# Kernel optimization log

Hardware: AMD Instinct MI355X
Metric: run time of the kernel (lower is better)

## Reference

```python
import jax, jax.numpy as jnp
import numpy as np

B, S, D_MODEL, H, D_KV = 16, 512, 768, 12, 64
EPS = 1e-6
ROPE_THETA = 10000.0


def rms_norm(x, w, eps=EPS):
    var = jnp.mean(jnp.square(x.astype(jnp.float32)), axis=-1, keepdims=True)
    return w * (x * jax.lax.rsqrt(var + eps))


def rotate_half(x):
    x1, x2 = jnp.split(x, 2, axis=-1)
    return jnp.concatenate([-x2, x1], axis=-1)


def build_rope(position_ids, inv_freq):
    # position_ids: [B,S] int; inv_freq: [d_kv/2]
    freqs = position_ids[:, :, None].astype(jnp.float32) * inv_freq[None, None, :]  # [B,S,d/2]
    emb = jnp.concatenate([freqs, freqs], axis=-1)  # [B,S,d_kv]
    return jnp.cos(emb), jnp.sin(emb)


def shape_heads(x, n_heads, d_kv):
    b, s, _ = x.shape
    return x.reshape(b, s, n_heads, d_kv).transpose(0, 2, 1, 3)  # [b,h,s,d]


def attend(h, norm_w, wq, wk, wv, wo, mask, cos=None, sin=None):
    # h: [b,s,d_model]; mask: [b,h,s,s] additive
    normed = rms_norm(h, norm_w)
    q = shape_heads(normed @ wq.T, H, D_KV)
    k = shape_heads(normed @ wk.T, H, D_KV)
    v = shape_heads(normed @ wv.T, H, D_KV)
    if cos is not None:
        c = cos[:, None, :, :]
        s = sin[:, None, :, :]
        q = q * c + rotate_half(q) * s
        k = k * c + rotate_half(k) * s
    # NOTE: kernel has no 1/sqrt(d) scaling
    scores = jnp.einsum('bhqd,bhkd->bhqk', q, k) + mask
    p = jax.nn.softmax(scores, axis=-1)
    out = jnp.einsum('bhqk,bhkd->bhqd', p, v)
    b, _, s, _ = out.shape
    out = out.transpose(0, 2, 1, 3).reshape(b, s, H * D_KV)
    return h + out @ wo.T


def setup_inputs() -> dict:
    key = jax.random.key(0)
    ks = jax.random.split(key, 12)
    scale = 1.0 / np.sqrt(D_MODEL)
    inp = {
        'hidden_states': jax.random.normal(ks[0], (B, S, D_MODEL), dtype=jnp.float32),
        'position_ids': jnp.broadcast_to(jnp.arange(S, dtype=jnp.int32)[None, :], (B, S)),
        'attention_mask': jnp.broadcast_to(
            jnp.where(jnp.arange(S)[None, :] <= jnp.arange(S)[:, None], 0.0, -1e9).astype(jnp.float32),
            (B, H, S, S)) + 0.0,
        'group_time_mask': jnp.zeros((S, H, B, B), dtype=jnp.float32),
        't_q': jax.random.normal(ks[1], (H * D_KV, D_MODEL), dtype=jnp.float32) * scale,
        't_k': jax.random.normal(ks[2], (H * D_KV, D_MODEL), dtype=jnp.float32) * scale,
        't_v': jax.random.normal(ks[3], (H * D_KV, D_MODEL), dtype=jnp.float32) * scale,
        't_o': jax.random.normal(ks[4], (D_MODEL, H * D_KV), dtype=jnp.float32) * scale,
        't_norm_w': jnp.ones((D_MODEL,), dtype=jnp.float32),
        'g_q': jax.random.normal(ks[5], (H * D_KV, D_MODEL), dtype=jnp.float32) * scale,
        'g_k': jax.random.normal(ks[6], (H * D_KV, D_MODEL), dtype=jnp.float32) * scale,
        'g_v': jax.random.normal(ks[7], (H * D_KV, D_MODEL), dtype=jnp.float32) * scale,
        'g_o': jax.random.normal(ks[8], (D_MODEL, H * D_KV), dtype=jnp.float32) * scale,
        'g_norm_w': jnp.ones((D_MODEL,), dtype=jnp.float32),
        'inv_freq': (1.0 / ROPE_THETA ** (jnp.arange(0, D_KV, 2, dtype=jnp.float32) / D_KV)),
    }
    return inp


def reference(hidden_states, position_ids, attention_mask, group_time_mask,
              t_q, t_k, t_v, t_o, t_norm_w,
              g_q, g_k, g_v, g_o, g_norm_w, inv_freq):
    cos, sin = build_rope(position_ids, inv_freq)
    h = attend(hidden_states, t_norm_w, t_q, t_k, t_v, t_o, attention_mask, cos, sin)
    h = h.transpose(1, 0, 2)  # [S,B,D]: group attention attends across groups
    h = attend(h, g_norm_w, g_q, g_k, g_v, g_o, group_time_mask)
    return h.transpose(1, 0, 2)
```

## Files before the change

### kernel.cpp

```cpp
#include <hip/hip_runtime.h>

#define DM   768
#define QKVN 2304
#define SQ   512
#define NB   16
#define NH   12

typedef unsigned short u16;
typedef _Float16 h16;
typedef _Float16 h16x8 __attribute__((ext_vector_type(8)));
typedef float f32x4 __attribute__((ext_vector_type(4)));

__device__ __forceinline__ u16 f2h(float f) {
  h16 h = (h16)f;
  return __builtin_bit_cast(u16, h);
}
__device__ __forceinline__ float h2f(u16 u) {
  return (float)__builtin_bit_cast(h16, u);
}
__device__ __forceinline__ void gload_lds16(const void* g, void* l) {
  __builtin_amdgcn_global_load_lds((__attribute__((address_space(1))) void*)(g),
                                   (__attribute__((address_space(3))) void*)(l), 16, 0, 0);
}

struct WPtrs { const float* s[8]; u16* d[8]; };
__global__ __launch_bounds__(256) void prep_k(WPtrs P, const float* __restrict__ invf,
                                              float* __restrict__ tab,
                                              const float* __restrict__ x,
                                              const float* __restrict__ tnw, const float* __restrict__ gnw,
                                              u16* __restrict__ xh, float* __restrict__ rs1) {
  const int bid = blockIdx.x, tid = threadIdx.x;
  if (bid < 4608) {
    int w = bid / 576;
    int i = ((bid % 576) * 256 + tid) * 4;
    float4 v = *reinterpret_cast<const float4*>(P.s[w] + i);
    if (w < 3 || (w >= 4 && w < 7)) {
      const float* nw = (w < 3) ? tnw : gnw;
      int k = i % 768;
      float4 f = *reinterpret_cast<const float4*>(nw + k);
      v.x *= f.x; v.y *= f.y; v.z *= f.z; v.w *= f.w;
    }
    ushort4 o;
    o.x = f2h(v.x); o.y = f2h(v.y); o.z = f2h(v.z); o.w = f2h(v.w);
    *reinterpret_cast<ushort4*>(P.d[w] + i) = o;
  } else if (bid < 4672) {
    int i = (bid - 4608) * 256 + tid;
    int pos = i >> 5, j = i & 31;
    float a = (float)pos * invf[j];
    float s, c;
    sincosf(a, &s, &c);
    tab[i * 2] = c; tab[i * 2 + 1] = s;
  } else {
    int wv = tid >> 6, lane = tid & 63;
    size_t t = (size_t)(bid - 4672) * 4 + wv;
    const float* row = x + t * DM;
    float4 v[3];
    float ss = 0.f;
#pragma unroll
    for (int i = 0; i < 3; i++) {
      v[i] = *reinterpret_cast<const float4*>(row + (lane + 64 * i) * 4);
      ss += v[i].x * v[i].x + v[i].y * v[i].y + v[i].z * v[i].z + v[i].w * v[i].w;
    }
#pragma unroll
    for (int d = 1; d < 64; d <<= 1) ss += __shfl_xor(ss, d);
    u16* orow = xh + t * DM;
#pragma unroll
    for (int i = 0; i < 3; i++) {
      int c = (lane + 64 * i) * 4;
      ushort4 o;
      o.x = f2h(v[i].x); o.y = f2h(v[i].y); o.z = f2h(v[i].z); o.w = f2h(v[i].w);
      *reinterpret_cast<ushort4*>(orow + c) = o;
    }
    if (lane == 0) rs1[t] = rsqrtf(ss * (1.0f / 768.f) + 1e-6f);
  }
}

__global__ __launch_bounds__(256) void rs2_k(const u16* __restrict__ x, float* __restrict__ rs2) {
  int wv = threadIdx.x >> 6, lane = threadIdx.x & 63;
  size_t t = (size_t)blockIdx.x * 4 + wv;
  const u16* row = x + t * DM;
  float ss = 0.f;
#pragma unroll
  for (int i = 0; i < 3; i++) {
    ushort4 rw = *reinterpret_cast<const ushort4*>(row + (lane + 64 * i) * 4);
    float a = h2f(rw.x), b = h2f(rw.y), c = h2f(rw.z), d = h2f(rw.w);
    ss += a * a + b * b + c * c + d * d;
  }
#pragma unroll
  for (int d = 1; d < 64; d <<= 1) ss += __shfl_xor(ss, d);
  if (lane == 0) rs2[t] = rsqrtf(ss * (1.0f / 768.f) + 1e-6f);
}

template <int CMODE, bool ROPE, int PERM, bool VT, bool RS>
__global__ __launch_bounds__(256, 3) void gemm_k(const u16* __restrict__ A, const u16* __restrict__ W, int N,
                                              void* __restrict__ C, const void* __restrict__ resid,
                                              const int* __restrict__ pids, const float* __restrict__ tab,
                                              u16* __restrict__ vt, const float* __restrict__ rsb) {
  __shared__ __align__(16) char L[3 * 16384];
  const int tid = threadIdx.x, w = tid >> 6, lane = tid & 63;
  const int wr = w >> 1, wc = w & 1;
  const int nbn = gridDim.y;
  int nf = blockIdx.y * gridDim.x + blockIdx.x;
  int nwg = gridDim.x * nbn;
  int swv = (nf & 7) * (nwg >> 3) + (nf >> 3);
  const int bm = swv / nbn;
  const int bnb = swv % nbn;
  const int l15 = lane & 15, l4 = lane >> 4;
  f32x4 acc[4][4] = {};

  const int r0 = tid >> 2, k40 = tid & 3;
  const int k4s = k40 ^ ((r0 >> 1) & 3);
  const size_t aA0 = (size_t)(bm * 128 + r0) * 1536 + k4s * 16;
  const size_t aA1 = (size_t)(bm * 128 + r0 + 64) * 1536 + k4s * 16;
  const size_t aB0 = (size_t)(bnb * 128 + r0) * 1536 + k4s * 16;
  const size_t aB1 = (size_t)(bnb * 128 + r0 + 64) * 1536 + k4s * 16;
  const int dc0 = tid * 16, dc1 = dc0 + 4096;
  const char* Ab = (const char*)A;
  const char* Wb = (const char*)W;

#define STAGE(T64, Q) do { \
    gload_lds16(Ab + aA0 + (T64), L + (Q) * 16384 + dc0); \
    gload_lds16(Ab + aA1 + (T64), L + (Q) * 16384 + dc1); \
    gload_lds16(Wb + aB0 + (T64), L + (Q) * 16384 + 8192 + dc0); \
    gload_lds16(Wb + aB1 + (T64), L + (Q) * 16384 + 8192 + dc1); \
  } while (0)

  int obA[4], obB[4];
#pragma unroll
  for (int i = 0; i < 4; i++) {
    int rowA = wr * 64 + i * 16 + l15;
    obA[i] = rowA * 64 + ((l4 ^ ((rowA >> 1) & 3)) * 16);
    int rowB = wc * 64 + i * 16 + l15;
    obB[i] = 8192 + rowB * 64 + ((l4 ^ ((rowB >> 1) & 3)) * 16);
  }

  STAGE(0, 0); STAGE(64, 1);
  asm volatile("s_waitcnt vmcnt(4)" ::: "memory");
  __builtin_amdgcn_sched_barrier(0);
  __builtin_amdgcn_s_barrier();
  __builtin_amdgcn_sched_barrier(0);

#pragma unroll
  for (int to = 0; to < 8; ++to) {
#pragma unroll
    for (int ti = 0; ti < 3; ++ti) {
      const int t = to * 3 + ti;
      const int tn = (t + 2 < 24) ? (t + 2) : 23;
      STAGE(tn * 64, (t + 2) % 3);
      const char* bq = L + (t % 3) * 16384;
      h16x8 am[4], bn[4];
#pragma unroll
      for (int i = 0; i < 4; i++) am[i] = *reinterpret_cast<const h16x8*>(bq + obA[i]);
#pragma unroll
      for (int j = 0; j < 4; j++) bn[j] = *reinterpret_cast<const h16x8*>(bq + obB[j]);
      __builtin_amdgcn_s_setprio(1);
#pragma unroll
      for (int i = 0; i < 4; i++)
#pragma unroll
        for (int j = 0; j < 4; j++)
          acc[i][j] = __builtin_amdgcn_mfma_f32_16x16x32_f16(am[i], bn[j], acc[i][j], 0, 0, 0);
      __builtin_amdgcn_s_setprio(0);
      asm volatile("s_waitcnt vmcnt(4)" ::: "memory");
      __builtin_amdgcn_sched_barrier(0);
      __builtin_amdgcn_s_barrier();
      __builtin_amdgcn_sched_barrier(0);
    }
  }
#undef STAGE
  asm volatile("s_waitcnt vmcnt(0)" ::: "memory");

  if (RS) {
#pragma unroll
    for (int i = 0; i < 4; i++) {
      int row0 = bm * 128 + wr * 64 + i * 16 + l4 * 4;
#pragma unroll
      for (int r = 0; r < 4; r++) {
        float s = rsb[row0 + r];
#pragma unroll
        for (int j = 0; j < 4; j++) acc[i][j][r] *= s;
      }
    }
  }

  if (VT && bnb >= 12) {
#pragma unroll
    for (int i = 0; i < 4; i++) {
      int row0 = bm * 128 + wr * 64 + i * 16 + l4 * 4;
      int b = row0 >> 9, s0 = row0 & 511;
#pragma unroll
      for (int j = 0; j < 4; j++) {
        int vcol = bnb * 128 + wc * 64 + j * 16 + l15 - 1536;
        int hh = vcol >> 6, dd = vcol & 63;
        u16* dst = vt + (((size_t)(b * NH + hh) * 64 + dd) << 9) + s0;
        ushort4 o;
        o.x = f2h(acc[i][j][0]); o.y = f2h(acc[i][j][1]);
        o.z = f2h(acc[i][j][2]); o.w = f2h(acc[i][j][3]);
        *reinterpret_cast<ushort4*>(dst) = o;
      }
    }
    return;
  }

  if (ROPE && bnb < 12) {
#pragma unroll
    for (int i = 0; i < 4; i++) {
      int row0 = bm * 128 + wr * 64 + i * 16 + l4 * 4;
#pragma unroll
      for (int r = 0; r < 4; r++) {
        int pos = pids[row0 + r];
        const float* tb = tab + pos * 64;
#pragma unroll
        for (int j = 0; j < 2; j++) {
          float2 cs = *reinterpret_cast<const float2*>(tb + 2 * (j * 16 + l15));
          float x1 = acc[i][j][r], x2 = acc[i][j + 2][r];
          acc[i][j][r]     = x1 * cs.x - x2 * cs.y;
          acc[i][j + 2][r] = x2 * cs.x + x1 * cs.y;
        }
      }
    }
  }
#pragma unroll
  for (int i = 0; i < 4; i++) {
    int row0 = bm * 128 + wr * 64 + i * 16 + l4 * 4;
#pragma unroll
    for (int j = 0; j < 4; j++) {
      int col = bnb * 128 + wc * 64 + j * 16 + l15;
#pragma unroll
      for (int r = 0; r < 4; r++) {
        int rr = row0 + r;
        int orow = (PERM == 0) ? rr : (PERM == 1) ? ((rr & 511) * 16 + (rr >> 9))
                                                  : ((rr & 15) * 512 + (rr >> 4));
        size_t idx = (size_t)orow * N + col;
        float v = acc[i][j][r];
        if (CMODE == 0)      ((u16*)C)[idx] = f2h(v);
        else if (CMODE == 1) ((u16*)C)[idx] = f2h(v + h2f(((const u16*)resid)[idx]));
        else                 ((float*)C)[idx] = v + h2f(((const u16*)resid)[idx]);
      }
    }
  }
}

__global__ __launch_bounds__(256) void attn1_k(const u16* __restrict__ qkv, const u16* __restrict__ vt,
                                               u16* __restrict__ O) {
  __shared__ __align__(16) char L[2][32768];
  __shared__ __align__(16) char Pl[4][4096];
  int nf = blockIdx.y * 8 + blockIdx.x;
  int swv = (nf & 7) * 192 + (nf >> 3);
  const int qt = swv & 7;
  const int bh = swv >> 3;
  const int b = bh / NH, h = bh % NH;
  const int tid = threadIdx.x, w = tid >> 6, lane = tid & 63;
  const int l15 = lane & 15, l4 = lane >> 4;
  const size_t qoff = ((size_t)(b * SQ + qt * 64 + w * 16 + l15)) * QKVN + h * 64;
  h16x8 qf[2];
  qf[0] = *reinterpret_cast<const h16x8*>(qkv + qoff + 8 * l4);
  qf[1] = *reinterpret_cast<const h16x8*>(qkv + qoff + 32 + 8 * l4);
  f32x4 acco[4] = {};
  float mrun[4] = {-3e38f, -3e38f, -3e38f, -3e38f};
  float lrun[4] = {0.f, 0.f, 0.f, 0.f};
  const int qrow = qt * 64 + w * 16 + l4 * 4;
  const int nkt = (qt >> 1) + 1;

  const u16* Kg = qkv + (size_t)b * SQ * QKVN + DM + h * 64;
  const int rK0 = tid >> 3;
  const size_t aK0 = (size_t)rK0 * QKVN + (size_t)(((tid & 7) ^ (rK0 & 7)) * 8);
  const u16* Vg = vt + (size_t)bh * 64 * SQ;
  const int dV0 = tid >> 4;
  const size_t aV0 = (size_t)dV0 * SQ + (size_t)(((tid & 15) ^ (dV0 & 15)) * 8);
  const int dst0 = tid * 16;

#define STAGE1(KT, BUF) do { \
    _Pragma("unroll") \
    for (int e = 0; e < 4; e++) \
      gload_lds16(Kg + aK0 + (size_t)e * (32 * QKVN) + (size_t)(KT) * (128 * QKVN), \
                  L[BUF] + dst0 + e * 4096); \
    _Pragma("unroll") \
    for (int e = 0; e < 4; e++) \
      gload_lds16(Vg + aV0 + e * (16 * SQ) + (KT) * 128, \
                  L[BUF] + 16384 + dst0 + e * 4096); \
  } while (0)

  STAGE1(0, 0);
  asm volatile("s_waitcnt vmcnt(0)" ::: "memory");
  __builtin_amdgcn_sched_barrier(0);
  __builtin_amdgcn_s_barrier();
  __builtin_amdgcn_sched_barrier(0);

  for (int kt = 0; kt < nkt; ++kt) {
    const int cur = kt & 1;
    if (kt + 1 < nkt) STAGE1(kt + 1, cur ^ 1);
    const char* Kb = L[cur];
    const char* Vb = L[cur] + 16384;
    f32x4 sc[8] = {};
    __builtin_amdgcn_s_setprio(1);
#pragma unroll
    for (int kk = 0; kk < 2; kk++) {
#pragma unroll
      for (int j = 0; j < 8; j++) {
        int row = j * 16 + l15;
        int off = row * 128 + (((kk * 4 + l4) ^ (row & 7)) * 16);
        h16x8 kf = *reinterpret_cast<const h16x8*>(Kb + off);
        sc[j] = __builtin_amdgcn_mfma_f32_16x16x32_f16(qf[kk], kf, sc[j], 0, 0, 0);
      }
    }
    __builtin_amdgcn_s_setprio(0);
    float pv[8][4];
#pragma unroll
    for (int j = 0; j < 8; j++)
#pragma unroll
      for (int r = 0; r < 4; r++) pv[j][r] = sc[j][r];
    if (kt == nkt - 1) {
#pragma unroll
      for (int r = 0; r < 4; r++) {
        int q = qrow + r;
#pragma unroll
        for (int j = 0; j < 8; j++) {
          int key = kt * 128 + j * 16 + l15;
          if (key > q) pv[j][r] = -1e30f;
        }
      }
    }
    float al[4];
#pragma unroll
    for (int r = 0; r < 4; r++) {
      float t0 = fmaxf(fmaxf(pv[0][r], pv[1][r]), fmaxf(pv[2][r], pv[3][r]));
      float t1 = fmaxf(fmaxf(pv[4][r], pv[5][r]), fmaxf(pv[6][r], pv[7][r]));
      float tm = fmaxf(t0, t1);
      tm = fmaxf(tm, __shfl_xor(tm, 1)); tm = fmaxf(tm, __shfl_xor(tm, 2));
      tm = fmaxf(tm, __shfl_xor(tm, 4)); tm = fmaxf(tm, __shfl_xor(tm, 8));
      float mn = fmaxf(mrun[r], tm);
      al[r] = __expf(mrun[r] - mn);
      mrun[r] = mn;
      float ts = 0.f;
#pragma unroll
      for (int j = 0; j < 8; j++) { float p = __expf(pv[j][r] - mn); pv[j][r] = p; ts += p; }
      ts += __shfl_xor(ts, 1); ts += __shfl_xor(ts, 2); ts += __shfl_xor(ts, 4); ts += __shfl_xor(ts, 8);
      lrun[r] = lrun[r] * al[r] + ts;
    }
#pragma unroll
    for (int j = 0; j < 4; j++)
#pragma unroll
      for (int r = 0; r < 4; r++) acco[j][r] *= al[r];
    char* pw = Pl[w];
#pragma unroll
    for (int r = 0; r < 4; r++) {
      int q = l4 * 4 + r;
#pragma unroll
      for (int j = 0; j < 8; j++) {
        int cw = j * 2 + (l15 >> 3);
        int byte = q * 256 + ((cw ^ (q & 15)) * 16) + (l15 & 7) * 2;
        *(u16*)(pw + byte) = f2h(pv[j][r]);
      }
    }
    asm volatile("s_waitcnt lgkmcnt(0)" ::: "memory");
    __builtin_amdgcn_sched_barrier(0);
    __builtin_amdgcn_s_setprio(1);
#pragma unroll
    for (int kk = 0; kk < 4; kk++) {
      h16x8 pa = *reinterpret_cast<const h16x8*>(pw + l15 * 256 + (((kk * 4 + l4) ^ l15) * 16));
#pragma unroll
      for (int j = 0; j < 4; j++) {
        int d = j * 16 + l15;
        int voff = d * 256 + (((kk * 4 + l4) ^ (d & 15)) * 16);
        h16x8 vf = *reinterpret_cast<const h16x8*>(Vb + voff);
        acco[j] = __builtin_amdgcn_mfma_f32_16x16x32_f16(pa, vf, acco[j], 0, 0, 0);
      }
    }
    __builtin_amdgcn_s_setprio(0);
    asm volatile("s_waitcnt vmcnt(0)" ::: "memory");
    __builtin_amdgcn_sched_barrier(0);
    __builtin_amdgcn_s_barrier();
    __builtin_amdgcn_sched_barrier(0);
  }
#undef STAGE1
#pragma unroll
  for (int r = 0; r < 4; r++) {
    float inv = 1.f / lrun[r];
    size_t orow = ((size_t)(b * SQ + qrow + r)) * DM + h * 64;
#pragma unroll
    for (int j = 0; j < 4; j++) O[orow + j * 16 + l15] = f2h(acco[j][r] * inv);
  }
}

__global__ __launch_bounds__(256) void attn2_k(const u16* __restrict__ qkv, const float* __restrict__ gmask,
                                               u16* __restrict__ O) {
  __shared__ float Pl[4][16][16];
  __shared__ float Vl[4][16][68];
  const int tid = threadIdx.x, w = tid >> 6, lane = tid & 63;
  const int idx = blockIdx.x * 4 + w;
  const int s = idx / NH, h = idx % NH;
  const int l15 = lane & 15, l4 = lane >> 4;
  const size_t base = ((size_t)(s * 16 + l15)) * QKVN + h * 64;
  h16x8 qf0 = *reinterpret_cast<const h16x8*>(qkv + base + 8 * l4);
  h16x8 qf1 = *reinterpret_cast<const h16x8*>(qkv + base + 32 + 8 * l4);
  h16x8 kf0 = *reinterpret_cast<const h16x8*>(qkv + base + DM + 8 * l4);
  h16x8 kf1 = *reinterpret_cast<const h16x8*>(qkv + base + DM + 32 + 8 * l4);
  f32x4 sc = {};
  sc = __builtin_amdgcn_mfma_f32_16x16x32_f16(qf0, kf0, sc, 0, 0, 0);
  sc = __builtin_amdgcn_mfma_f32_16x16x32_f16(qf1, kf1, sc, 0, 0, 0);
  {
    int key = lane >> 2, d0 = (lane & 3) * 16;
    const u16* vsrc = qkv + ((size_t)(s * 16 + key)) * QKVN + 2 * DM + h * 64 + d0;
#pragma unroll
    for (int i = 0; i < 16; i += 4) {
      ushort4 vv = *reinterpret_cast<const ushort4*>(vsrc + i);
      Vl[w][key][d0 + i + 0] = h2f(vv.x);
      Vl[w][key][d0 + i + 1] = h2f(vv.y);
      Vl[w][key][d0 + i + 2] = h2f(vv.z);
      Vl[w][key][d0 + i + 3] = h2f(vv.w);
    }
  }
  const float* gm = gmask + ((size_t)s * NH + h) * 256;
#pragma unroll
  for (int r = 0; r < 4; r++) {
    float v = sc[r] + gm[(l4 * 4 + r) * 16 + l15];
    float mx = v;
    mx = fmaxf(mx, __shfl_xor(mx, 1)); mx = fmaxf(mx, __shfl_xor(mx, 2));
    mx = fmaxf(mx, __shfl_xor(mx, 4)); mx = fmaxf(mx, __shfl_xor(mx, 8));
    float p = __expf(v - mx);
    float su = p;
    su += __shfl_xor(su, 1); su += __shfl_xor(su, 2); su += __shfl_xor(su, 4); su += __shfl_xor(su, 8);
    Pl[w][l4 * 4 + r][l15] = p / su;
  }
  asm volatile("s_waitcnt lgkmcnt(0)" ::: "memory");
  __builtin_amdgcn_sched_barrier(0);
  const int q = lane >> 2, d0 = (lane & 3) * 16;
  float o[16] = {};
#pragma unroll
  for (int key = 0; key < 16; key++) {
    float pp = Pl[w][q][key];
#pragma unroll
    for (int dd = 0; dd < 16; dd += 4) {
      float4 vv = *reinterpret_cast<const float4*>(&Vl[w][key][d0 + dd]);
      o[dd + 0] += pp * vv.x; o[dd + 1] += pp * vv.y; o[dd + 2] += pp * vv.z; o[dd + 3] += pp * vv.w;
    }
  }
  u16* orow = O + ((size_t)(s * 16 + q)) * DM + h * 64 + d0;
#pragma unroll
  for (int i = 0; i < 16; i += 4) {
    ushort4 ov;
    ov.x = f2h(o[i]); ov.y = f2h(o[i + 1]); ov.z = f2h(o[i + 2]); ov.w = f2h(o[i + 3]);
    *reinterpret_cast<ushort4*>(orow + i) = ov;
  }
}

extern "C" void kernel_launch(void* const* d_in, const int* in_sizes, int n_in,
                              void* d_out, int out_size, void* d_ws, size_t ws_size,
                              hipStream_t stream) {
  const float* hidden = (const float*)d_in[0];
  const int*   pids   = (const int*)d_in[1];
  const float* gmask  = (const float*)d_in[3];
  const float* tq = (const float*)d_in[4];
  const float* tk = (const float*)d_in[5];
  const float* tv = (const float*)d_in[6];
  const float* to_ = (const float*)d_in[7];
  const float* tnw = (const float*)d_in[8];
  const float* gq = (const float*)d_in[9];
  const float* gk = (const float*)d_in[10];
  const float* gv = (const float*)d_in[11];
  const float* go = (const float*)d_in[12];
  const float* gnw = (const float*)d_in[13];
  const float* invf = (const float*)d_in[14];
  float* out = (float*)d_out;
  char* ws = (char*)d_ws;

  u16*   wq1    = (u16*)(ws);
  u16*   wo1    = (u16*)(ws + 3538944);
  u16*   wq2    = (u16*)(ws + 4718592);
  u16*   wo2    = (u16*)(ws + 8257536);
  float* tab    = (float*)(ws + 9437184);
  u16*   xh     = (u16*)(ws + 9568256);
  u16*   obuf   = (u16*)(ws + 22151168);
  u16*   h1     = (u16*)(ws + 34734080);
  u16*   qkv    = (u16*)(ws + 59899904);
  u16*   vt     = (u16*)(ws + 97648640);
  float* rs1    = (float*)(ws + 110231552);
  float* rs2    = (float*)(ws + 110264320);

  const int WN = 768 * 768;
  WPtrs P;
  P.s[0] = tq;  P.d[0] = wq1;
  P.s[1] = tk;  P.d[1] = wq1 + WN;
  P.s[2] = tv;  P.d[2] = wq1 + 2 * WN;
  P.s[3] = to_; P.d[3] = wo1;
  P.s[4] = gq;  P.d[4] = wq2;
  P.s[5] = gk;  P.d[5] = wq2 + WN;
  P.s[6] = gv;  P.d[6] = wq2 + 2 * WN;
  P.s[7] = go;  P.d[7] = wo2;

  prep_k<<<6720, 256, 0, stream>>>(P, invf, tab, hidden, tnw, gnw, xh, rs1);
  gemm_k<0, true, 0, true, true><<<dim3(64, 18), 256, 0, stream>>>(xh, wq1, QKVN, qkv, nullptr, pids, tab, vt, rs1);
  attn1_k<<<dim3(8, 192), 256, 0, stream>>>(qkv, vt, obuf);
  gemm_k<1, false, 0, false, false><<<dim3(64, 6), 256, 0, stream>>>(obuf, wo1, DM, h1, xh, nullptr, nullptr, nullptr, nullptr);

  rs2_k<<<2048, 256, 0, stream>>>(h1, rs2);
  gemm_k<0, false, 1, false, true><<<dim3(64, 18), 256, 0, stream>>>(h1, wq2, QKVN, qkv, nullptr, nullptr, nullptr, nullptr, rs2);
  attn2_k<<<1536, 256, 0, stream>>>(qkv, gmask, obuf);
  gemm_k<2, false, 2, false, false><<<dim3(64, 6), 256, 0, stream>>>(obuf, wo2, DM, out, h1, nullptr, nullptr, nullptr, nullptr);
}
```

Before: 197.0 us.

## Halve GEMM M-tile and fuse second RMS-norm sum-of-squares into O-projection epilogue

Shrinks the GEMM block tile from 128x128 to 64x128, doubling grid size and raising the occupancy bound to 4 blocks per CU. The standalone rs2 reduction kernel is removed: the first output-projection GEMM accumulates per-row sums of squares via shuffles and atomicAdd into a buffer zeroed in prep_k. The following QKV GEMM then computes rsqrt from that buffer. This cuts one launch and a full pass over h1, at the cost of atomics and more redundant weight-tile loads from the smaller M tile.

Result: slower. 219.0 us (+11.2%).

```diff
diff --git a/kernel.cpp b/kernel.cpp
--- a/kernel.cpp
+++ b/kernel.cpp
@@ -28,7 +28,8 @@
                                               float* __restrict__ tab,
                                               const float* __restrict__ x,
                                               const float* __restrict__ tnw, const float* __restrict__ gnw,
-                                              u16* __restrict__ xh, float* __restrict__ rs1) {
+                                              u16* __restrict__ xh, float* __restrict__ rs1,
+                                              float* __restrict__ ssq) {
   const int bid = blockIdx.x, tid = threadIdx.x;
   if (bid < 4608) {
     int w = bid / 576;
@@ -50,6 +51,7 @@
     float s, c;
     sincosf(a, &s, &c);
     tab[i * 2] = c; tab[i * 2 + 1] = s;
+    if (i < 8192) ssq[i] = 0.f;
   } else {
     int wv = tid >> 6, lane = tid & 63;
     size_t t = (size_t)(bid - 4672) * 4 + wv;
@@ -75,28 +77,13 @@
   }
 }
 
-__global__ __launch_bounds__(256) void rs2_k(const u16* __restrict__ x, float* __restrict__ rs2) {
-  int wv = threadIdx.x >> 6, lane = threadIdx.x & 63;
-  size_t t = (size_t)blockIdx.x * 4 + wv;
-  const u16* row = x + t * DM;
-  float ss = 0.f;
-#pragma unroll
-  for (int i = 0; i < 3; i++) {
-    ushort4 rw = *reinterpret_cast<const ushort4*>(row + (lane + 64 * i) * 4);
-    float a = h2f(rw.x), b = h2f(rw.y), c = h2f(rw.z), d = h2f(rw.w);
-    ss += a * a + b * b + c * c + d * d;
-  }
-#pragma unroll
-  for (int d = 1; d < 64; d <<= 1) ss += __shfl_xor(ss, d);
-  if (lane == 0) rs2[t] = rsqrtf(ss * (1.0f / 768.f) + 1e-6f);
-}
-
-template <int CMODE, bool ROPE, int PERM, bool VT, bool RS>
-__global__ __launch_bounds__(256, 3) void gemm_k(const u16* __restrict__ A, const u16* __restrict__ W, int N,
+template <int CMODE, bool ROPE, int PERM, bool VT, int RSMODE, bool SSQ>
+__global__ __launch_bounds__(256, 4) void gemm_k(const u16* __restrict__ A, const u16* __restrict__ W, int N,
                                               void* __restrict__ C, const void* __restrict__ resid,
                                               const int* __restrict__ pids, const float* __restrict__ tab,
-                                              u16* __restrict__ vt, const float* __restrict__ rsb) {
-  __shared__ __align__(16) char L[3 * 16384];
+                                              u16* __restrict__ vt, const float* __restrict__ rsb,
+                                              float* __restrict__ ssq) {
+  __shared__ __align__(16) char L[3 * 12288];
   const int tid = threadIdx.x, w = tid >> 6, lane = tid & 63;
   const int wr = w >> 1, wc = w & 1;
   const int nbn = gridDim.y;
@@ -106,36 +93,37 @@
   const int bm = swv / nbn;
   const int bnb = swv % nbn;
   const int l15 = lane & 15, l4 = lane >> 4;
-  f32x4 acc[4][4] = {};
+  f32x4 acc[2][4] = {};
 
   const int r0 = tid >> 2, k40 = tid & 3;
   const int k4s = k40 ^ ((r0 >> 1) & 3);
-  const size_t aA0 = (size_t)(bm * 128 + r0) * 1536 + k4s * 16;
-  const size_t aA1 = (size_t)(bm * 128 + r0 + 64) * 1536 + k4s * 16;
+  const size_t aA0 = (size_t)(bm * 64 + r0) * 1536 + k4s * 16;
   const size_t aB0 = (size_t)(bnb * 128 + r0) * 1536 + k4s * 16;
   const size_t aB1 = (size_t)(bnb * 128 + r0 + 64) * 1536 + k4s * 16;
-  const int dc0 = tid * 16, dc1 = dc0 + 4096;
+  const int dcA = tid * 16, dcB0 = 4096 + tid * 16, dcB1 = 8192 + tid * 16;
   const char* Ab = (const char*)A;
   const char* Wb = (const char*)W;
 
 #define STAGE(T64, Q) do { \
-    gload_lds16(Ab + aA0 + (T64), L + (Q) * 16384 + dc0); \
-    gload_lds16(Ab + aA1 + (T64), L + (Q) * 16384 + dc1); \
-    gload_lds16(Wb + aB0 + (T64), L + (Q) * 16384 + 8192 + dc0); \
-    gload_lds16(Wb + aB1 + (T64), L + (Q) * 16384 + 8192 + dc1); \
+    gload_lds16(Ab + aA0 + (T64), L + (Q) * 12288 + dcA); \
+    gload_lds16(Wb + aB0 + (T64), L + (Q) * 12288 + dcB0); \
+    gload_lds16(Wb + aB1 + (T64), L + (Q) * 12288 + dcB1); \
   } while (0)
 
-  int obA[4], obB[4];
-#pragma unroll
-  for (int i = 0; i < 4; i++) {
-    int rowA = wr * 64 + i * 16 + l15;
+  int obA[2], obB[4];
+#pragma unroll
+  for (int i = 0; i < 2; i++) {
+    int rowA = wr * 32 + i * 16 + l15;
     obA[i] = rowA * 64 + ((l4 ^ ((rowA >> 1) & 3)) * 16);
-    int rowB = wc * 64 + i * 16 + l15;
-    obB[i] = 8192 + rowB * 64 + ((l4 ^ ((rowB >> 1) & 3)) * 16);
+  }
+#pragma unroll
+  for (int j = 0; j < 4; j++) {
+    int rowB = wc * 64 + j * 16 + l15;
+    obB[j] = 4096 + rowB * 64 + ((l4 ^ ((rowB >> 1) & 3)) * 16);
   }
 
   STAGE(0, 0); STAGE(64, 1);
-  asm volatile("s_waitcnt vmcnt(4)" ::: "memory");
+  asm volatile("s_waitcnt vmcnt(3)" ::: "memory");
   __builtin_amdgcn_sched_barrier(0);
   __builtin_amdgcn_s_barrier();
   __builtin_amdgcn_sched_barrier(0);
@@ -147,20 +135,20 @@
       const int t = to * 3 + ti;
       const int tn = (t + 2 < 24) ? (t + 2) : 23;
       STAGE(tn * 64, (t + 2) % 3);
-      const char* bq = L + (t % 3) * 16384;
-      h16x8 am[4], bn[4];
-#pragma unroll
-      for (int i = 0; i < 4; i++) am[i] = *reinterpret_cast<const h16x8*>(bq + obA[i]);
+      const char* bq = L + (t % 3) * 12288;
+      h16x8 am[2], bn[4];
+#pragma unroll
+      for (int i = 0; i < 2; i++) am[i] = *reinterpret_cast<const h16x8*>(bq + obA[i]);
 #pragma unroll
       for (int j = 0; j < 4; j++) bn[j] = *reinterpret_cast<const h16x8*>(bq + obB[j]);
       __builtin_amdgcn_s_setprio(1);
 #pragma unroll
-      for (int i = 0; i < 4; i++)
+      for (int i = 0; i < 2; i++)
 #pragma unroll
         for (int j = 0; j < 4; j++)
           acc[i][j] = __builtin_amdgcn_mfma_f32_16x16x32_f16(am[i], bn[j], acc[i][j], 0, 0, 0);
       __builtin_amdgcn_s_setprio(0);
-      asm volatile("s_waitcnt vmcnt(4)" ::: "memory");
+      asm volatile("s_waitcnt vmcnt(3)" ::: "memory");
       __builtin_amdgcn_sched_barrier(0);
       __builtin_amdgcn_s_barrier();
       __builtin_amdgcn_sched_barrier(0);
@@ -169,13 +157,14 @@
 #undef STAGE
   asm volatile("s_waitcnt vmcnt(0)" ::: "memory");
 
-  if (RS) {
-#pragma unroll
-    for (int i = 0; i < 4; i++) {
-      int row0 = bm * 128 + wr * 64 + i * 16 + l4 * 4;
+  if (RSMODE) {
+#pragma unroll
+    for (int i = 0; i < 2; i++) {
+      int row0 = bm * 64 + wr * 32 + i * 16 + l4 * 4;
 #pragma unroll
       for (int r = 0; r < 4; r++) {
-        float s = rsb[row0 + r];
+        float s = (RSMODE == 1) ? rsb[row0 + r]
+                                : rsqrtf(rsb[row0 + r] * (1.0f / 768.f) + 1e-6f);
 #pragma unroll
         for (int j = 0; j < 4; j++) acc[i][j][r] *= s;
       }
@@ -184,8 +173,8 @@
 
   if (VT && bnb >= 12) {
 #pragma unroll
-    for (int i = 0; i < 4; i++) {
-      int row0 = bm * 128 + wr * 64 + i * 16 + l4 * 4;
+    for (int i = 0; i < 2; i++) {
+      int row0 = bm * 64 + wr * 32 + i * 16 + l4 * 4;
       int b = row0 >> 9, s0 = row0 & 511;
 #pragma unroll
       for (int j = 0; j < 4; j++) {
@@ -203,8 +192,8 @@
 
   if (ROPE && bnb < 12) {
 #pragma unroll
-    for (int i = 0; i < 4; i++) {
-      int row0 = bm * 128 + wr * 64 + i * 16 + l4 * 4;
+    for (int i = 0; i < 2; i++) {
+      int row0 = bm * 64 + wr * 32 + i * 16 + l4 * 4;
 #pragma unroll
       for (int r = 0; r < 4; r++) {
         int pos = pids[row0 + r];
@@ -220,21 +209,28 @@
     }
   }
 #pragma unroll
-  for (int i = 0; i < 4; i++) {
-    int row0 = bm * 128 + wr * 64 + i * 16 + l4 * 4;
-#pragma unroll
-    for (int j = 0; j < 4; j++) {
-      int col = bnb * 128 + wc * 64 + j * 16 + l15;
-#pragma unroll
-      for (int r = 0; r < 4; r++) {
-        int rr = row0 + r;
-        int orow = (PERM == 0) ? rr : (PERM == 1) ? ((rr & 511) * 16 + (rr >> 9))
-                                                  : ((rr & 15) * 512 + (rr >> 4));
+  for (int i = 0; i < 2; i++) {
+    int row0 = bm * 64 + wr * 32 + i * 16 + l4 * 4;
+#pragma unroll
+    for (int r = 0; r < 4; r++) {
+      int rr = row0 + r;
+      int orow = (PERM == 0) ? rr : (PERM == 1) ? ((rr & 511) * 16 + (rr >> 9))
+                                                : ((rr & 15) * 512 + (rr >> 4));
+      float sq = 0.f;
+#pragma unroll
+      for (int j = 0; j < 4; j++) {
+        int col = bnb * 128 + wc * 64 + j * 16 + l15;
         size_t idx = (size_t)orow * N + col;
         float v = acc[i][j][r];
         if (CMODE == 0)      ((u16*)C)[idx] = f2h(v);
-        else if (CMODE == 1) ((u16*)C)[idx] = f2h(v + h2f(((const u16*)resid)[idx]));
+        else if (CMODE == 1) { v += h2f(((const u16*)resid)[idx]); ((u16*)C)[idx] = f2h(v); }
         else                 ((float*)C)[idx] = v + h2f(((const u16*)resid)[idx]);
+        if (SSQ) sq += v * v;
+      }
+      if (SSQ) {
+        sq += __shfl_xor(sq, 1); sq += __shfl_xor(sq, 2);
+        sq += __shfl_xor(sq, 4); sq += __shfl_xor(sq, 8);
+        if (l15 == 0) atomicAdd(&ssq[rr], sq);
       }
     }
   }
@@ -475,7 +471,7 @@
   u16*   qkv    = (u16*)(ws + 59899904);
   u16*   vt     = (u16*)(ws + 97648640);
   float* rs1    = (float*)(ws + 110231552);
-  float* rs2    = (float*)(ws + 110264320);
+  float* ssq    = (float*)(ws + 110264320);
 
   const int WN = 768 * 768;
   WPtrs P;
@@ -488,13 +484,12 @@
   P.s[6] = gv;  P.d[6] = wq2 + 2 * WN;
   P.s[7] = go;  P.d[7] = wo2;
 
-  prep_k<<<6720, 256, 0, stream>>>(P, invf, tab, hidden, tnw, gnw, xh, rs1);
-  gemm_k<0, true, 0, true, true><<<dim3(64, 18), 256, 0, stream>>>(xh, wq1, QKVN, qkv, nullptr, pids, tab, vt, rs1);
+  prep_k<<<6720, 256, 0, stream>>>(P, invf, tab, hidden, tnw, gnw, xh, rs1, ssq);
+  gemm_k<0, true, 0, true, 1, false><<<dim3(128, 18), 256, 0, stream>>>(xh, wq1, QKVN, qkv, nullptr, pids, tab, vt, rs1, nullptr);
   attn1_k<<<dim3(8, 192), 256, 0, stream>>>(qkv, vt, obuf);
-  gemm_k<1, false, 0, false, false><<<dim3(64, 6), 256, 0, stream>>>(obuf, wo1, DM, h1, xh, nullptr, nullptr, nullptr, nullptr);
-
-  rs2_k<<<2048, 256, 0, stream>>>(h1, rs2);
-  gemm_k<0, false, 1, false, true><<<dim3(64, 18), 256, 0, stream>>>(h1, wq2, QKVN, qkv, nullptr, nullptr, nullptr, nullptr, rs2);
+  gemm_k<1, false, 0, false, 0, true><<<dim3(128, 6), 256, 0, stream>>>(obuf, wo1, DM, h1, xh, nullptr, nullptr, nullptr, nullptr, ssq);
+
+  gemm_k<0, false, 1, false, 2, false><<<dim3(128, 18), 256, 0, stream>>>(h1, wq2, QKVN, qkv, nullptr, nullptr, nullptr, nullptr, ssq, nullptr);
   attn2_k<<<1536, 256, 0, stream>>>(qkv, gmask, obuf);
-  gemm_k<2, false, 2, false, false><<<dim3(64, 6), 256, 0, stream>>>(obuf, wo2, DM, out, h1, nullptr, nullptr, nullptr, nullptr);
-}
+  gemm_k<2, false, 2, false, 0, false><<<dim3(128, 6), 256, 0, stream>>>(obuf, wo2, DM, out, h1, nullptr, nullptr, nullptr, nullptr, nullptr);
+}
```
